# Kernel optimization log

Hardware: AMD Instinct MI355X
Metric: run time of the kernel (lower is better)

## Reference

```python
import jax, jax.numpy as jnp
import numpy as np
import math

EPS = 1e-11

def _gaussian_kernel3():
    # fixed 3x3 gaussian, mean=(3-1)/2=1, variance=0.5^2
    coords = jnp.arange(3, dtype=jnp.float32)
    xg = jnp.tile(coords[None, :], (3, 1))  # x_cord.repeat(3).view(3,3)
    yg = xg.T
    variance = 0.25
    g = (1.0 / (2.0 * math.pi * variance)) * jnp.exp(-((xg - 1.0) ** 2 + (yg - 1.0) ** 2) / (2.0 * variance))
    return g  # (3,3)

def setup_inputs() -> dict:
    key = jax.random.key(0)
    k1, k2 = jax.random.split(key)
    b, cin, h, w = 8, 512, 16, 16
    cout = 128
    x = jax.random.normal(k1, (b, cin, h, w), dtype=jnp.float32)
    w_conv = jax.random.normal(k2, (cout, cin), dtype=jnp.float32) * (1.0 / np.sqrt(cin))
    return {"x": x, "w_conv": w_conv}

def reference(x, w_conv):
    # 1x1 conv (no bias) + relu
    y = jnp.einsum('bihw,oi->bohw', x, w_conv)
    y = jax.nn.relu(y)
    # depthwise 3x3 gaussian blur, VALID padding (matches nn.Conv2d default padding=0)
    c = w_conv.shape[0]
    gk = _gaussian_kernel3()
    dw = jnp.tile(gk[None, None], (c, 1, 1, 1))  # (C,1,3,3)
    y = jax.lax.conv_general_dilated(
        y, dw, window_strides=(1, 1), padding='VALID',
        dimension_numbers=('NCHW', 'OIHW', 'NCHW'), feature_group_count=c)
    b, c, h, w = y.shape
    hw = h * w
    xf = y.reshape(b, c, hw)
    # shifted copies: xs[b, ch, i, p] = xf[b, ch, (p - i) mod hw]
    p = jnp.arange(hw)
    idx = (p[None, :] - p[:, None]) % hw  # (hw_i, hw_p)
    xs = xf[:, :, idx]  # [b, c, hw, hw]
    # responses[b, ch1, ch2, p] = sum_i xf[b,ch1,i] * xf[b,ch2,(p-i)%hw]
    R = jnp.einsum('bai,bcip->bacp', xf, xs)  # [b, c, c, hw]
    # faithful torch reshape: [b, c, c*hw] -> view(b, hw, c*c), max over dim 1
    resp = R.reshape(b, hw, c * c)
    c_ij = jnp.sqrt(jnp.max(resp, axis=1))  # [b, c*c]
    norm = jnp.sum(c_ij ** 2, axis=1, keepdims=True) + EPS
    return c_ij / norm
```

## Files before the change

kernel.cpp:

```cpp
#include <hip/hip_runtime.h>
#include <hip/hip_bf16.h>

typedef __bf16 bf16x8 __attribute__((ext_vector_type(8)));
typedef float floatx4 __attribute__((ext_vector_type(4)));
typedef unsigned short u16;
typedef unsigned int u32;

#define HW 196
#define NB 8
#define NC 128
#define CL 480
#define WROW 12544

#define OFF_XFRSW 0
#define OFF_XFE   458752
#define OFF_W     8323072
#define OFF_Y     21168160
#define OFF_XBT   22216736
#define OFF_WB    24313888
#define OFF_PARTS 24444960

__global__ __launch_bounds__(256) void k_cast(const float* __restrict__ x,
                                              const float* __restrict__ wc,
                                              u16* __restrict__ xbT,
                                              u16* __restrict__ wb) {
  const int bid = blockIdx.x;
  const int t   = threadIdx.x;
  if (bid < 512) {
    const int gid = bid * 256 + t;
    const int pix = gid & 255;
    const int kc  = (gid >> 8) & 63;
    const int b   = gid >> 14;
    union { u16 u[8]; uint4 v; } pk;
#pragma unroll
    for (int j = 0; j < 8; ++j) {
      union { __hip_bfloat16 h; u16 u; } cv;
      cv.h = __float2bfloat16(x[((size_t)(b * 512 + kc * 8 + j)) * 256 + pix]);
      pk.u[j] = cv.u;
    }
    ((uint4*)xbT)[(size_t)(b * 256 + pix) * 64 + kc] = pk.v;
  } else {
    const int wid = (bid - 512) * 256 + t;
    const float4* wf4 = (const float4*)wc;
    const float4 f0 = wf4[wid * 2], f1 = wf4[wid * 2 + 1];
    union { u16 u[8]; uint4 v; } pk;
    union { __hip_bfloat16 h; u16 u; } cv;
    cv.h = __float2bfloat16(f0.x); pk.u[0] = cv.u;
    cv.h = __float2bfloat16(f0.y); pk.u[1] = cv.u;
    cv.h = __float2bfloat16(f0.z); pk.u[2] = cv.u;
    cv.h = __float2bfloat16(f0.w); pk.u[3] = cv.u;
    cv.h = __float2bfloat16(f1.x); pk.u[4] = cv.u;
    cv.h = __float2bfloat16(f1.y); pk.u[5] = cv.u;
    cv.h = __float2bfloat16(f1.z); pk.u[6] = cv.u;
    cv.h = __float2bfloat16(f1.w); pk.u[7] = cv.u;
    ((uint4*)wb)[wid] = pk.v;
  }
}

__global__ __launch_bounds__(256) void k_conv(const u16* __restrict__ xbT,
                                              const u16* __restrict__ wb,
                                              float* __restrict__ Y) {
  const int b  = blockIdx.x;
  const int pt = blockIdx.y;
  const int t  = threadIdx.x;
  const int lane = t & 63, wv = t >> 6;
  const int n = lane & 15, quad = lane >> 4;
  const int pix = pt * 16 + n;

  const u16* xrow = xbT + ((size_t)(b * 256) + pix) * 512 + quad * 8;
  const u16* wrow = wb + (size_t)n * 512 + quad * 8;

  floatx4 acc[2];
  acc[0] = (floatx4){0.f, 0.f, 0.f, 0.f};
  acc[1] = (floatx4){0.f, 0.f, 0.f, 0.f};

#pragma unroll
  for (int kb = 0; kb < 16; ++kb) {
    const bf16x8 bv = *(const bf16x8*)(xrow + kb * 32);
#pragma unroll
    for (int j = 0; j < 2; ++j) {
      const int at = wv * 2 + j;
      const bf16x8 av = *(const bf16x8*)(wrow + (size_t)(at * 16) * 512 + kb * 32);
      acc[j] = __builtin_amdgcn_mfma_f32_16x16x32_bf16(av, bv, acc[j], 0, 0, 0);
    }
  }

  float* Yb = Y + ((size_t)b * 128) * 256 + pix;
#pragma unroll
  for (int j = 0; j < 2; ++j)
#pragma unroll
    for (int rr = 0; rr < 4; ++rr)
      Yb[((wv * 2 + j) * 16 + quad * 4 + rr) * 256] = fmaxf(acc[j][rr], 0.f);
}

__global__ __launch_bounds__(256) void k_blur(const float* __restrict__ Y,
                                              uint4* __restrict__ xfr_sw,
                                              u16* __restrict__ xfe) {
  const int b  = blockIdx.x;
  const int rg = blockIdx.y;
  const int t  = threadIdx.x;

  __shared__ float ybuf[4][256];
  __shared__ u16 ydup[4][592];

#pragma unroll
  for (int oo = 0; oo < 4; ++oo)
    ybuf[oo][t] = Y[((size_t)(b * 128) + rg * 4 + oo) * 256 + t];
  __syncthreads();

  const float GC = 0.63661977236758138f;
  const float GE = GC * 0.13533528323661270f;
  const float GD = GC * 0.018315638888734179f;

  if (t < HW) {
    const int h = t / 14, w2 = t - h * 14;
#pragma unroll
    for (int oo = 0; oo < 4; ++oo) {
      const float* yb = &ybuf[oo][h * 16 + w2];
      float v = GD * (yb[0] + yb[2] + yb[32] + yb[34])
              + GE * (yb[1] + yb[16] + yb[18] + yb[33])
              + GC * yb[17];
      union { __hip_bfloat16 h2; u16 u; } cv; cv.h2 = __float2bfloat16(v);
      ydup[oo][t] = cv.u; ydup[oo][t + 196] = cv.u; ydup[oo][t + 392] = cv.u;
    }
  }
  __syncthreads();

  if (t < 112) {
    const int oo = t / 28;
    const int g  = t - oo * 28;
    const int kb = g >> 2, quad = g & 3;
    const int c  = rg * 4 + oo;
    const int at = c >> 4, m = c & 15;
    union { u16 u[8]; uint4 v; } pk;
#pragma unroll
    for (int j = 0; j < 8; ++j) {
      const int k = g * 8 + j;
      pk.u[j] = (k < HW) ? ydup[oo][HW - k] : (u16)0;
    }
    xfr_sw[b * 3584 + ((kb * 8 + at) * 4 + quad) * 16 + m] = pk.v;
  }

  uint4* xfe4 = (uint4*)xfe;
  for (int idx = t; idx < 4 * 8 * 60; idx += 256) {
    const int oo = idx / 480;
    const int rem = idx - oo * 480;
    const int S = rem / 60;
    const int g = rem - S * 60;
    const int c = rg * 4 + oo;
    union { u16 u[8]; uint4 v; } pk;
#pragma unroll
    for (int j = 0; j < 8; ++j) pk.u[j] = ydup[oo][g * 8 + j + S];
    xfe4[((size_t)(b * NC + c) * 8 + S) * 60 + g] = pk.v;
  }
}

__global__ __launch_bounds__(256, 2) void k_cooc(const uint4* __restrict__ xfr_sw,
                                                 const u16* __restrict__ xfe,
                                                 u32* __restrict__ W) {
  const int b     = blockIdx.x;
  const int cpair = blockIdx.y;
  const int t     = threadIdx.x;

  __shared__ __align__(16) uint4 Abuf[3584];
  __shared__ __align__(16) u16 Obuf[32 * 200];

  {
    const uint4* src = xfr_sw + b * 3584;
    for (int j = t; j < 3584; j += 256) Abuf[j] = src[j];
  }
  __syncthreads();

  const int lane = t & 63;
  const int wv   = t >> 6;
  const int n    = lane & 15;
  const int quad = lane >> 4;
  const u16* xbase = xfe + ((size_t)(b * NC) * 8) * CL + (n & 8) + quad * 8
                   + (size_t)(n & 7) * CL;

  for (int c2 = 0; c2 < 2; ++c2) {
    const int c = cpair * 2 + c2;
    const u16* xc = xbase + (size_t)c * (8 * CL);

    floatx4 acc[8][4];
#pragma unroll
    for (int at = 0; at < 8; ++at)
#pragma unroll
      for (int j = 0; j < 4; ++j) acc[at][j] = (floatx4){0.f, 0.f, 0.f, 0.f};

    for (int kb = 0; kb < 7; ++kb) {
      bf16x8 af[8];
#pragma unroll
      for (int at = 0; at < 8; ++at)
        af[at] = *((const bf16x8*)&Abuf[(kb * 8 + at) * 64 + lane]);

#define DO_PT(JC)                                                                \
      {                                                                          \
        const int p0 = (wv + 4 * (JC)) * 16;                                     \
        const bf16x8 bv = *((const bf16x8*)&xc[p0 + kb * 32]);                   \
        _Pragma("unroll")                                                        \
        for (int at = 0; at < 8; ++at)                                           \
          acc[at][JC] = __builtin_amdgcn_mfma_f32_16x16x32_bf16(af[at], bv,      \
                                                                acc[at][JC], 0, 0, 0); \
      }
      DO_PT(0)
      DO_PT(1)
      DO_PT(2)
      if (wv == 0) { DO_PT(3) }
#undef DO_PT
    }

#define EPI(JC)                                                                  \
    {                                                                            \
      const int p = (wv + 4 * (JC)) * 16 + n;                                    \
      if (p < HW) {                                                              \
        _Pragma("unroll")                                                        \
        for (int a0t = 0; a0t < 2; ++a0t) {                                      \
          _Pragma("unroll")                                                      \
          for (int rr = 0; rr < 4; ++rr) {                                       \
            float v = fmaxf(fmaxf(acc[a0t][JC][rr], acc[a0t + 2][JC][rr]),       \
                            fmaxf(acc[a0t + 4][JC][rr], acc[a0t + 6][JC][rr]));  \
            const int a1 = a0t * 16 + quad * 4 + rr;                             \
            union { __hip_bfloat16 h; u16 u; } cv;                               \
            cv.h = __float2bfloat16(v);                                          \
            Obuf[a1 * 200 + p] = cv.u;                                           \
          }                                                                      \
        }                                                                        \
      }                                                                          \
    }
    EPI(0)
    EPI(1)
    EPI(2)
    if (wv == 0) { EPI(3) }
#undef EPI
    __syncthreads();

    {
      const u32* O32 = (const u32*)Obuf;
      u32* Wb = W + ((size_t)b * 32) * WROW + c * 98;
      for (int j = t; j < 32 * 98; j += 256) {
        const int row = (int)(((unsigned)j * 10700u) >> 20);
        const int col = j - row * 98;
        Wb[row * WROW + col] = O32[row * 100 + col];
      }
    }
    __syncthreads();
  }
}

__device__ __forceinline__ float blo(u32 v) { return __uint_as_float(v << 16); }
__device__ __forceinline__ float bhi(u32 v) { return __uint_as_float(v & 0xffff0000u); }

__global__ __launch_bounds__(256) void k_max(const u32* __restrict__ W,
                                             float* __restrict__ out,
                                             float* __restrict__ parts) {
  const int t = threadIdx.x;
  const int wv = t >> 6, lane = t & 63;
  const int g = lane >> 4, ol = lane & 15;
  const int octet = blockIdx.x * 64 + wv * 16 + ol;
  const int b  = octet >> 11;
  const int r0 = (octet & 2047) << 3;
  const uint4* Wb = (const uint4*)(W + (size_t)b * 32 * WROW);

  float m[8];
#pragma unroll
  for (int j = 0; j < 8; ++j) m[j] = 0.f;

#pragma unroll
  for (int k = 0; k < 8; ++k) {
    const int a1 = g * 8 + k;
    const int s = (r0 - ((a1 * 8704) & 16383)) & 16383;
    const uint4 v = Wb[(a1 * WROW + (s >> 1)) >> 2];
    m[0] = fmaxf(m[0], blo(v.x)); m[1] = fmaxf(m[1], bhi(v.x));
    m[2] = fmaxf(m[2], blo(v.y)); m[3] = fmaxf(m[3], bhi(v.y));
    m[4] = fmaxf(m[4], blo(v.z)); m[5] = fmaxf(m[5], bhi(v.z));
    m[6] = fmaxf(m[6], blo(v.w)); m[7] = fmaxf(m[7], bhi(v.w));
    if (s < 8704) {
      const uint4 v2 = Wb[((a1 * WROW + (s >> 1)) >> 2) + 2048];
      m[0] = fmaxf(m[0], blo(v2.x)); m[1] = fmaxf(m[1], bhi(v2.x));
      m[2] = fmaxf(m[2], blo(v2.y)); m[3] = fmaxf(m[3], bhi(v2.y));
      m[4] = fmaxf(m[4], blo(v2.z)); m[5] = fmaxf(m[5], bhi(v2.z));
      m[6] = fmaxf(m[6], blo(v2.w)); m[7] = fmaxf(m[7], bhi(v2.w));
    }
  }

#pragma unroll
  for (int j = 0; j < 8; ++j) {
    m[j] = fmaxf(m[j], __shfl_xor(m[j], 16, 64));
    m[j] = fmaxf(m[j], __shfl_xor(m[j], 32, 64));
  }

  float s2 = 0.f;
  if (g == 0) {
    float4 s0, s1;
    s0.x = sqrtf(m[0]); s0.y = sqrtf(m[1]); s0.z = sqrtf(m[2]); s0.w = sqrtf(m[3]);
    s1.x = sqrtf(m[4]); s1.y = sqrtf(m[5]); s1.z = sqrtf(m[6]); s1.w = sqrtf(m[7]);
    float4* op = (float4*)(out + (size_t)octet * 8);
    op[0] = s0; op[1] = s1;
    s2 = ((m[0] + m[1]) + (m[2] + m[3])) + ((m[4] + m[5]) + (m[6] + m[7]));
  }

#pragma unroll
  for (int off = 32; off > 0; off >>= 1) s2 += __shfl_down(s2, off, 64);
  __shared__ float part[4];
  if (lane == 0) part[wv] = s2;
  __syncthreads();
  if (t == 0)
    parts[blockIdx.x] = part[0] + part[1] + part[2] + part[3];
}

__global__ __launch_bounds__(256) void k_norm(const float* __restrict__ parts,
                                              float* __restrict__ out) {
  const int b = blockIdx.x >> 6;
  const int gid = blockIdx.x * 256 + threadIdx.x;
  float s = 0.f;
#pragma unroll
  for (int i = 0; i < 32; ++i) s += parts[b * 32 + i];
  out[gid] = out[gid] / (s + 1e-11f);
}

extern "C" void kernel_launch(void* const* d_in, const int* in_sizes, int n_in,
                              void* d_out, int out_size, void* d_ws, size_t ws_size,
                              hipStream_t stream) {
  const float* x  = (const float*)d_in[0];
  const float* wc = (const float*)d_in[1];

  char* ws = (char*)d_ws;
  uint4* xfr_sw = (uint4*)(ws + OFF_XFRSW);
  u16*   xfe    = (u16*)(ws + OFF_XFE);
  u32*   W      = (u32*)(ws + OFF_W);
  float* Y      = (float*)(ws + OFF_Y);
  u16*   xbT    = (u16*)(ws + OFF_XBT);
  u16*   wb     = (u16*)(ws + OFF_WB);
  float* parts  = (float*)(ws + OFF_PARTS);

  k_cast<<<544, 256, 0, stream>>>(x, wc, xbT, wb);
  k_conv<<<dim3(NB, 16), 256, 0, stream>>>(xbT, wb, Y);
  k_blur<<<dim3(NB, 32), 256, 0, stream>>>(Y, xfr_sw, xfe);
  k_cooc<<<dim3(NB, 64), 256, 0, stream>>>(xfr_sw, xfe, W);
  k_max<<<256, 256, 0, stream>>>(W, (float*)d_out, parts);
  k_norm<<<(NB * 16384) / 256, 256, 0, stream>>>(parts, (float*)d_out);
}
```

Baseline: 108.3 us.

## Fuse 1x1 conv and gaussian blur into one kernel via shared memory

Merges the conv and blur kernels so each block computes a 16-channel by 256-pixel conv tile with MFMA, keeps the ReLU output in shared memory, and blurs and repacks it there. This drops the Y round trip through global memory and one kernel launch. In exchange the grid shrinks from 128+256 blocks to 64 blocks of 512 threads, which lowers parallelism, and shared-memory use per block grows.

```diff
diff --git a/kernel.cpp b/kernel.cpp
--- a/kernel.cpp
+++ b/kernel.cpp
@@ -57,18 +57,22 @@
   }
 }
 
-__global__ __launch_bounds__(256) void k_conv(const u16* __restrict__ xbT,
-                                              const u16* __restrict__ wb,
-                                              float* __restrict__ Y) {
+__global__ __launch_bounds__(512) void k_convblur(const u16* __restrict__ xbT,
+                                                  const u16* __restrict__ wb,
+                                                  uint4* __restrict__ xfr_sw,
+                                                  u16* __restrict__ xfe) {
   const int b  = blockIdx.x;
-  const int pt = blockIdx.y;
+  const int og = blockIdx.y;
   const int t  = threadIdx.x;
   const int lane = t & 63, wv = t >> 6;
   const int n = lane & 15, quad = lane >> 4;
-  const int pix = pt * 16 + n;
-
-  const u16* xrow = xbT + ((size_t)(b * 256) + pix) * 512 + quad * 8;
-  const u16* wrow = wb + (size_t)n * 512 + quad * 8;
+
+  __shared__ float ybuf[16][260];
+  __shared__ u16 ydup[16][592];
+
+  const u16* wrow  = wb + (size_t)(og * 16 + n) * 512 + quad * 8;
+  const u16* xrow0 = xbT + ((size_t)(b * 256) + (wv * 2) * 16 + n) * 512 + quad * 8;
+  const u16* xrow1 = xrow0 + 16 * 512;
 
   floatx4 acc[2];
   acc[0] = (floatx4){0.f, 0.f, 0.f, 0.f};
@@ -76,36 +80,18 @@
 
 #pragma unroll
   for (int kb = 0; kb < 16; ++kb) {
-    const bf16x8 bv = *(const bf16x8*)(xrow + kb * 32);
-#pragma unroll
-    for (int j = 0; j < 2; ++j) {
-      const int at = wv * 2 + j;
-      const bf16x8 av = *(const bf16x8*)(wrow + (size_t)(at * 16) * 512 + kb * 32);
-      acc[j] = __builtin_amdgcn_mfma_f32_16x16x32_bf16(av, bv, acc[j], 0, 0, 0);
-    }
-  }
-
-  float* Yb = Y + ((size_t)b * 128) * 256 + pix;
+    const bf16x8 av  = *(const bf16x8*)(wrow  + kb * 32);
+    const bf16x8 bv0 = *(const bf16x8*)(xrow0 + kb * 32);
+    const bf16x8 bv1 = *(const bf16x8*)(xrow1 + kb * 32);
+    acc[0] = __builtin_amdgcn_mfma_f32_16x16x32_bf16(av, bv0, acc[0], 0, 0, 0);
+    acc[1] = __builtin_amdgcn_mfma_f32_16x16x32_bf16(av, bv1, acc[1], 0, 0, 0);
+  }
+
 #pragma unroll
   for (int j = 0; j < 2; ++j)
 #pragma unroll
     for (int rr = 0; rr < 4; ++rr)
-      Yb[((wv * 2 + j) * 16 + quad * 4 + rr) * 256] = fmaxf(acc[j][rr], 0.f);
-}
-
-__global__ __launch_bounds__(256) void k_blur(const float* __restrict__ Y,
-                                              uint4* __restrict__ xfr_sw,
-                                              u16* __restrict__ xfe) {
-  const int b  = blockIdx.x;
-  const int rg = blockIdx.y;
-  const int t  = threadIdx.x;
-
-  __shared__ float ybuf[4][256];
-  __shared__ u16 ydup[4][592];
-
-#pragma unroll
-  for (int oo = 0; oo < 4; ++oo)
-    ybuf[oo][t] = Y[((size_t)(b * 128) + rg * 4 + oo) * 256 + t];
+      ybuf[quad * 4 + rr][(wv * 2 + j) * 16 + n] = fmaxf(acc[j][rr], 0.f);
   __syncthreads();
 
   const float GC = 0.63661977236758138f;
@@ -115,7 +101,7 @@
   if (t < HW) {
     const int h = t / 14, w2 = t - h * 14;
 #pragma unroll
-    for (int oo = 0; oo < 4; ++oo) {
+    for (int oo = 0; oo < 16; ++oo) {
       const float* yb = &ybuf[oo][h * 16 + w2];
       float v = GD * (yb[0] + yb[2] + yb[32] + yb[34])
               + GE * (yb[1] + yb[16] + yb[18] + yb[33])
@@ -126,28 +112,26 @@
   }
   __syncthreads();
 
-  if (t < 112) {
+  if (t < 448) {
     const int oo = t / 28;
     const int g  = t - oo * 28;
-    const int kb = g >> 2, quad = g & 3;
-    const int c  = rg * 4 + oo;
-    const int at = c >> 4, m = c & 15;
+    const int kb = g >> 2, qd = g & 3;
     union { u16 u[8]; uint4 v; } pk;
 #pragma unroll
     for (int j = 0; j < 8; ++j) {
       const int k = g * 8 + j;
       pk.u[j] = (k < HW) ? ydup[oo][HW - k] : (u16)0;
     }
-    xfr_sw[b * 3584 + ((kb * 8 + at) * 4 + quad) * 16 + m] = pk.v;
+    xfr_sw[b * 3584 + ((kb * 8 + og) * 4 + qd) * 16 + oo] = pk.v;
   }
 
   uint4* xfe4 = (uint4*)xfe;
-  for (int idx = t; idx < 4 * 8 * 60; idx += 256) {
+  for (int idx = t; idx < 16 * 8 * 60; idx += 512) {
     const int oo = idx / 480;
     const int rem = idx - oo * 480;
     const int S = rem / 60;
     const int g = rem - S * 60;
-    const int c = rg * 4 + oo;
+    const int c = og * 16 + oo;
     union { u16 u[8]; uint4 v; } pk;
 #pragma unroll
     for (int j = 0; j < 8; ++j) pk.u[j] = ydup[oo][g * 8 + j + S];
@@ -329,14 +313,12 @@
   uint4* xfr_sw = (uint4*)(ws + OFF_XFRSW);
   u16*   xfe    = (u16*)(ws + OFF_XFE);
   u32*   W      = (u32*)(ws + OFF_W);
-  float* Y      = (float*)(ws + OFF_Y);
   u16*   xbT    = (u16*)(ws + OFF_XBT);
   u16*   wb     = (u16*)(ws + OFF_WB);
   float* parts  = (float*)(ws + OFF_PARTS);
 
   k_cast<<<544, 256, 0, stream>>>(x, wc, xbT, wb);
-  k_conv<<<dim3(NB, 16), 256, 0, stream>>>(xbT, wb, Y);
-  k_blur<<<dim3(NB, 32), 256, 0, stream>>>(Y, xfr_sw, xfe);
+  k_convblur<<<dim3(NB, 8), 512, 0, stream>>>(xbT, wb, xfr_sw, xfe);
   k_cooc<<<dim3(NB, 64), 256, 0, stream>>>(xfr_sw, xfe, W);
   k_max<<<256, 256, 0, stream>>>(W, (float*)d_out, parts);
   k_norm<<<(NB * 16384) / 256, 256, 0, stream>>>(parts, (float*)d_out);
```

Measured after the change: 114.7 us. 1.06x slower.
